# Optimization experiments

Measured on AMD Instinct MI355X. Metric: run time of the kernel, lower is better.

## Reference

```python
import jax, jax.numpy as jnp
import numpy as np

# Model constants (match init_kwargs / torchcde conventions)
B = 1024        # batch
L = 128         # number of spline knots (grid_points = 0..L-1)
C_IN = 8        # input_channels
HID = 64        # hidden_channels
MLP_H = 128     # CDEFunc hidden width
INIT_H = 20     # initial-network hidden width


def setup_inputs() -> dict:
    key = jax.random.key(0)
    ks = jax.random.split(key, 9)
    # cubic spline coeffs: (B, L-1, 4*C_IN) laid out as [a, b, c, d] per interval
    coeffs = jax.random.normal(ks[0], (B, L - 1, 4 * C_IN), dtype=jnp.float32) * 0.1
    # initial network: C_IN -> 20 -> HID (ReLU, then Tanh)
    Wi1 = jax.random.normal(ks[1], (C_IN, INIT_H), dtype=jnp.float32) / np.sqrt(C_IN)
    bi1 = jnp.zeros((INIT_H,), jnp.float32)
    Wi2 = jax.random.normal(ks[2], (INIT_H, HID), dtype=jnp.float32) / np.sqrt(INIT_H)
    bi2 = jnp.zeros((HID,), jnp.float32)
    # CDE vector field: (HID+1) -> 128 -> C_IN*HID (ReLU, then Tanh)
    W1 = jax.random.normal(ks[3], (HID + 1, MLP_H), dtype=jnp.float32) / np.sqrt(HID + 1)
    b1 = jnp.zeros((MLP_H,), jnp.float32)
    W2 = jax.random.normal(ks[4], (MLP_H, C_IN * HID), dtype=jnp.float32) / np.sqrt(MLP_H)
    b2 = jnp.zeros((C_IN * HID,), jnp.float32)
    return {"coeffs": coeffs, "Wi1": Wi1, "bi1": bi1, "Wi2": Wi2, "bi2": bi2,
            "W1": W1, "b1": b1, "W2": W2, "b2": b2}


def reference(coeffs, Wi1, bi1, Wi2, bi2, W1, b1, W2, b2):
    Lm1 = coeffs.shape[1]
    # a,b,c,d: each (B, L-1, C_IN). X(t) = a + b*f + c*f^2 + d*f^3 on interval idx,
    # dX/dt = b + 2c*f + 3d*f^2, with f = t - idx (torchcde CubicSpline convention).
    a, b, c, d = jnp.split(coeffs, 4, axis=-1)

    def dXdt(t):
        idx = jnp.clip(jnp.floor(t).astype(jnp.int32), 0, Lm1 - 1)
        fr = t - idx
        return b[:, idx] + 2.0 * c[:, idx] * fr + 3.0 * d[:, idx] * fr * fr  # (B, C_IN)

    def cde_func(t, z):
        # FFN([HID+1, 128, C_IN*HID], ReLU hidden, Tanh output) on concat(t, z)
        tz = jnp.concatenate([jnp.full((z.shape[0], 1), t, z.dtype), z], axis=1)
        h = jax.nn.relu(tz @ W1 + b1)
        return jnp.tanh(h @ W2 + b2).reshape(z.shape[0], HID, C_IN)  # (B, HID, C_IN)

    def vf(t, z):
        # dz/dt = f(t,z) @ dX/dt
        return jnp.einsum('bhc,bc->bh', cde_func(t, z), dXdt(t))

    # z0 = initial(X(t0)); X(0) = a at interval 0 with frac 0
    X0 = a[:, 0]
    z0 = jnp.tanh(jax.nn.relu(X0 @ Wi1 + bi1) @ Wi2 + bi2)  # (B, HID)

    def rk4_step(z, i):
        t = i.astype(z.dtype)
        k1 = vf(t, z)
        k2 = vf(t + 0.5, z + 0.5 * k1)
        k3 = vf(t + 0.5, z + 0.5 * k2)
        k4 = vf(t + 1.0, z + k3)
        z_new = z + (k1 + 2.0 * k2 + 2.0 * k3 + k4) / 6.0
        return z_new, z_new

    _, zs = jax.lax.scan(rk4_step, z0, jnp.arange(Lm1))  # (L-1, B, HID)
    # z evaluated at all grid points, like cdeint(t=X.grid_points): (B, L, HID)
    return jnp.concatenate([z0[None], zs], axis=0).transpose(1, 0, 2)
```

## Files before the change

kernel.cpp:

```cpp
#include <hip/hip_runtime.h>
#include <stdint.h>

#define LM1   127
#define NTHR  256

typedef _Float16 half2_t __attribute__((ext_vector_type(2)));
typedef _Float16 half8_t __attribute__((ext_vector_type(8)));
typedef float    f32x4  __attribute__((ext_vector_type(4)));

__device__ __forceinline__ float fdot2(uint32_t a, uint32_t b, float c) {
  return __builtin_amdgcn_fdot2(__builtin_bit_cast(half2_t, a),
                                __builtin_bit_cast(half2_t, b), c, false);
}
__device__ __forceinline__ uint32_t packh2(float a, float b) {
  half2_t h = {(_Float16)a, (_Float16)b};
  return __builtin_bit_cast(uint32_t, h);
}
__device__ __forceinline__ float fast_tanh(float x) {
  float e = __expf(2.0f * x);
  return 1.0f - 2.0f * __builtin_amdgcn_rcpf(e + 1.0f);
}

__global__ void __launch_bounds__(NTHR, 1) cde_kernel(
    const float* __restrict__ coeffs,
    const float* __restrict__ Wi1, const float* __restrict__ bi1,
    const float* __restrict__ Wi2, const float* __restrict__ bi2,
    const float* __restrict__ W1,  const float* __restrict__ b1,
    const float* __restrict__ W2,  const float* __restrict__ b2,
    float* __restrict__ out)
{
  __shared__ _Float16 hA[16 * 136];
  __shared__ _Float16 zsb[4 * 64];
  __shared__ float    fbuf[4 * 576];
  __shared__ float    gds[3][4][8];

  const int t    = threadIdx.x;
  const int lane = t & 63;
  const int w    = t >> 6;
  const int r    = lane & 3;
  const int hxl  = lane >> 2;
  const int hx   = w * 16 + hxl;
  const int row0 = blockIdx.x * 4;

  {
    uint32_t* h32 = (uint32_t*)hA;
    for (int u = t; u < 16 * 136 / 2; u += NTHR) h32[u] = 0u;
  }

  const int j2 = 2 * lane;
  uint32_t w1A[32], w1B[32];
  #pragma unroll 8
  for (int m = 0; m < 32; ++m) {
    w1A[m] = packh2(W1[(1 + 2 * m) * 128 + j2],     W1[(2 + 2 * m) * 128 + j2]);
    w1B[m] = packh2(W1[(1 + 2 * m) * 128 + j2 + 1], W1[(2 + 2 * m) * 128 + j2 + 1]);
  }
  const float w1t0 = W1[j2], w1t1 = W1[j2 + 1];
  const float b10  = b1[j2], b11  = b1[j2 + 1];

  float b2r[8];
  #pragma unroll
  for (int c = 0; c < 8; ++c) b2r[c] = b2[hx * 8 + c];

  half8_t bf[8][4];
  {
    const int ncol = w * 128 + (lane & 15);
    const int kq   = (lane >> 4) * 8;
    #pragma unroll
    for (int nt = 0; nt < 8; ++nt)
      #pragma unroll
      for (int kt = 0; kt < 4; ++kt)
        #pragma unroll
        for (int j = 0; j < 8; ++j)
          bf[nt][kt][j] = (_Float16)W2[(kt * 32 + kq + j) * 512 + ncol + nt * 16];
  }

  float z;
  {
    const float* cb = coeffs + (size_t)(row0 + r) * (LM1 * 32);
    float x0[8];
    #pragma unroll
    for (int c = 0; c < 8; ++c) x0[c] = cb[c];
    float acc = bi2[hx];
    for (int j = 0; j < 20; ++j) {
      float u = bi1[j];
      #pragma unroll
      for (int c = 0; c < 8; ++c) u += x0[c] * Wi1[c * 20 + j];
      u = fmaxf(u, 0.0f);
      acc += u * Wi2[j * 64 + hx];
    }
    z = fast_tanh(acc);
  }
  out[(size_t)(row0 + r) * 8192 + hx] = z;

  float* const fw = fbuf + w * 576;

  for (int i = 0; i < LM1; ++i) {
    __syncthreads();
    if (t < 32) {
      const int rg = t >> 3, cg = t & 7;
      const float* cb = coeffs + (size_t)(row0 + rg) * (LM1 * 32) + (size_t)i * 32;
      const float bb = cb[8 + cg], cc = cb[16 + cg], dd = cb[24 + cg];
      gds[0][rg][cg] = bb;
      gds[1][rg][cg] = bb + cc + 0.75f * dd;
      gds[2][rg][cg] = (i < LM1 - 1) ? cb[32 + 8 + cg]
                                     : (bb + 2.0f * cc + 3.0f * dd);
    }

    float ksum = 0.0f, kprev = 0.0f;
    #pragma unroll
    for (int s = 0; s < 4; ++s) {
      const float coef = (s == 0) ? 0.0f : (s == 3) ? 1.0f : 0.5f;
      const float ts   = (float)i + ((s == 0) ? 0.0f : (s == 3) ? 1.0f : 0.5f);
      const int   gi   = (s == 0) ? 0 : (s == 3) ? 2 : 1;

      zsb[r * 64 + hx] = (_Float16)(z + coef * kprev);
      __syncthreads();

      {
        uint32_t zz[32];
        const uint4* zq = (const uint4*)(zsb + w * 64);
        #pragma unroll
        for (int q = 0; q < 8; ++q) {
          uint4 v = zq[q];
          zz[4 * q] = v.x; zz[4 * q + 1] = v.y; zz[4 * q + 2] = v.z; zz[4 * q + 3] = v.w;
        }
        float a0 = ts * w1t0 + b10, a1 = ts * w1t1 + b11;
        float a0b = 0.0f, a1b = 0.0f;
        #pragma unroll
        for (int m = 0; m < 32; m += 2) {
          a0  = fdot2(w1A[m],     zz[m],     a0);
          a1  = fdot2(w1B[m],     zz[m],     a1);
          a0b = fdot2(w1A[m + 1], zz[m + 1], a0b);
          a1b = fdot2(w1B[m + 1], zz[m + 1], a1b);
        }
        const float h0 = fmaxf(a0 + a0b, 0.0f);
        const float h1 = fmaxf(a1 + a1b, 0.0f);
        *(uint32_t*)(hA + w * 136 + 2 * lane) = packh2(h0, h1);
      }
      __syncthreads();

      {
        uint4 afu[4];
        const _Float16* hap = hA + (lane & 15) * 136 + (lane >> 4) * 8;
        #pragma unroll
        for (int kt = 0; kt < 4; ++kt)
          afu[kt] = *(const uint4*)(hap + kt * 32);

        f32x4 dacc[8];
        #pragma unroll
        for (int np = 0; np < 4; ++np) {
          f32x4 d0 = {0.f, 0.f, 0.f, 0.f};
          f32x4 d1 = {0.f, 0.f, 0.f, 0.f};
          #pragma unroll
          for (int kt = 0; kt < 4; ++kt) {
            half8_t a = __builtin_bit_cast(half8_t, afu[kt]);
            d0 = __builtin_amdgcn_mfma_f32_16x16x32_f16(a, bf[2 * np][kt],     d0, 0, 0, 0);
            d1 = __builtin_amdgcn_mfma_f32_16x16x32_f16(a, bf[2 * np + 1][kt], d1, 0, 0, 0);
          }
          dacc[2 * np] = d0; dacc[2 * np + 1] = d1;
        }
        if (lane < 16) {
          #pragma unroll
          for (int nt = 0; nt < 8; ++nt) {
            const int cl = nt * 16 + lane;
            *(f32x4*)(fw + 4 * cl + 4 * (cl >> 3)) = dacc[nt];
          }
        }
      }
      asm volatile("s_waitcnt lgkmcnt(0)" ::: "memory");

      {
        const f32x4 ga = *(const f32x4*)&gds[gi][r][0];
        const f32x4 gb4 = *(const f32x4*)&gds[gi][r][4];
        const float gg[8] = {ga.x, ga.y, ga.z, ga.w, gb4.x, gb4.y, gb4.z, gb4.w};
        const float* fr_ = fw + 36 * hxl + r;
        float kcv = 0.0f;
        #pragma unroll
        for (int c = 0; c < 8; ++c)
          kcv += fast_tanh(fr_[4 * c] + b2r[c]) * gg[c];
        kprev = kcv;
        ksum += ((s == 1 || s == 2) ? 2.0f : 1.0f) * kcv;
      }
    }
    z += ksum * (1.0f / 6.0f);
    out[(size_t)(row0 + r) * 8192 + (size_t)(i + 1) * 64 + hx] = z;
  }
}

extern "C" void kernel_launch(void* const* d_in, const int* in_sizes, int n_in,
                              void* d_out, int out_size, void* d_ws, size_t ws_size,
                              hipStream_t stream) {
  const float* coeffs = (const float*)d_in[0];
  const float* Wi1    = (const float*)d_in[1];
  const float* bi1    = (const float*)d_in[2];
  const float* Wi2    = (const float*)d_in[3];
  const float* bi2    = (const float*)d_in[4];
  const float* W1     = (const float*)d_in[5];
  const float* b1     = (const float*)d_in[6];
  const float* W2     = (const float*)d_in[7];
  const float* b2     = (const float*)d_in[8];
  float* out          = (float*)d_out;
  (void)in_sizes; (void)n_in; (void)out_size; (void)d_ws; (void)ws_size;
  cde_kernel<<<256, NTHR, 0, stream>>>(coeffs, Wi1, bi1, Wi2, bi2,
                                       W1, b1, W2, b2, out);
}
```

Baseline: 659.2 us.

## Split work across 8 waves and compute the first layer with MFMA

Raises the block to 512 threads (8 waves), so each wave owns 64 output columns of the second GEMM and 8 hidden units for the state update. The first layer is moved from fdot2 loops to MFMA over a zero-padded 16-row z tile. The spline coefficient loads are prefetched one step ahead into double-buffered shared memory, which removes a barrier per step. Half of the lanes now sit idle during the tanh/contraction phase, and the first MFMA spends 12 of its 16 rows on padding.

Result: faster. 595.0 us (-9.7%).

```diff
diff --git a/kernel.cpp b/kernel.cpp
--- a/kernel.cpp
+++ b/kernel.cpp
@@ -1,27 +1,18 @@
 #include <hip/hip_runtime.h>
 #include <stdint.h>
 
-#define LM1   127
-#define NTHR  256
+#define LM1  127
+#define NTHR 512
 
-typedef _Float16 half2_t __attribute__((ext_vector_type(2)));
 typedef _Float16 half8_t __attribute__((ext_vector_type(8)));
-typedef float    f32x4  __attribute__((ext_vector_type(4)));
+typedef float    f32x4   __attribute__((ext_vector_type(4)));
 
-__device__ __forceinline__ float fdot2(uint32_t a, uint32_t b, float c) {
-  return __builtin_amdgcn_fdot2(__builtin_bit_cast(half2_t, a),
-                                __builtin_bit_cast(half2_t, b), c, false);
-}
-__device__ __forceinline__ uint32_t packh2(float a, float b) {
-  half2_t h = {(_Float16)a, (_Float16)b};
-  return __builtin_bit_cast(uint32_t, h);
-}
 __device__ __forceinline__ float fast_tanh(float x) {
   float e = __expf(2.0f * x);
   return 1.0f - 2.0f * __builtin_amdgcn_rcpf(e + 1.0f);
 }
 
-__global__ void __launch_bounds__(NTHR, 1) cde_kernel(
+__global__ void __launch_bounds__(NTHR, 2) cde_kernel(
     const float* __restrict__ coeffs,
     const float* __restrict__ Wi1, const float* __restrict__ bi1,
     const float* __restrict__ Wi2, const float* __restrict__ bi2,
@@ -29,53 +20,50 @@
     const float* __restrict__ W2,  const float* __restrict__ b2,
     float* __restrict__ out)
 {
-  __shared__ _Float16 hA[16 * 136];
-  __shared__ _Float16 zsb[4 * 64];
-  __shared__ float    fbuf[4 * 576];
-  __shared__ float    gds[3][4][8];
+  __shared__ _Float16 zsb[16 * 72];
+  __shared__ _Float16 hA [16 * 136];
+  __shared__ float    fwb[8][284];
+  __shared__ float    gds[2][3][4][8];
 
   const int t    = threadIdx.x;
   const int lane = t & 63;
   const int w    = t >> 6;
+  const int l15  = lane & 15;
+  const int lq   = lane >> 4;
   const int r    = lane & 3;
-  const int hxl  = lane >> 2;
-  const int hx   = w * 16 + hxl;
+  const int hxl  = (lane >> 2) & 7;
+  const int hx   = w * 8 + hxl;
   const int row0 = blockIdx.x * 4;
+  const bool owner = (lane < 32);
 
-  {
-    uint32_t* h32 = (uint32_t*)hA;
-    for (int u = t; u < 16 * 136 / 2; u += NTHR) h32[u] = 0u;
-  }
+  for (int u = t; u < 16 * 72 / 2;  u += NTHR) ((uint32_t*)zsb)[u] = 0u;
+  for (int u = t; u < 16 * 136 / 2; u += NTHR) ((uint32_t*)hA)[u]  = 0u;
 
-  const int j2 = 2 * lane;
-  uint32_t w1A[32], w1B[32];
-  #pragma unroll 8
-  for (int m = 0; m < 32; ++m) {
-    w1A[m] = packh2(W1[(1 + 2 * m) * 128 + j2],     W1[(2 + 2 * m) * 128 + j2]);
-    w1B[m] = packh2(W1[(1 + 2 * m) * 128 + j2 + 1], W1[(2 + 2 * m) * 128 + j2 + 1]);
-  }
-  const float w1t0 = W1[j2], w1t1 = W1[j2 + 1];
-  const float b10  = b1[j2], b11  = b1[j2 + 1];
+  half8_t bB[2];
+  #pragma unroll
+  for (int kt = 0; kt < 2; ++kt)
+    #pragma unroll
+    for (int j = 0; j < 8; ++j)
+      bB[kt][j] = (_Float16)W1[(1 + kt * 32 + lq * 8 + j) * 128 + w * 16 + l15];
+  const float w1t_c = W1[w * 16 + l15];
+  const float b1_c  = b1[w * 16 + l15];
+
+  half8_t bf[4][4];
+  #pragma unroll
+  for (int nt = 0; nt < 4; ++nt)
+    #pragma unroll
+    for (int kt = 0; kt < 4; ++kt)
+      #pragma unroll
+      for (int j = 0; j < 8; ++j)
+        bf[nt][kt][j] =
+            (_Float16)W2[(kt * 32 + lq * 8 + j) * 512 + w * 64 + nt * 16 + l15];
 
   float b2r[8];
   #pragma unroll
   for (int c = 0; c < 8; ++c) b2r[c] = b2[hx * 8 + c];
 
-  half8_t bf[8][4];
-  {
-    const int ncol = w * 128 + (lane & 15);
-    const int kq   = (lane >> 4) * 8;
-    #pragma unroll
-    for (int nt = 0; nt < 8; ++nt)
-      #pragma unroll
-      for (int kt = 0; kt < 4; ++kt)
-        #pragma unroll
-        for (int j = 0; j < 8; ++j)
-          bf[nt][kt][j] = (_Float16)W2[(kt * 32 + kq + j) * 512 + ncol + nt * 16];
-  }
-
-  float z;
-  {
+  float z = 0.0f;
+  if (owner) {
     const float* cb = coeffs + (size_t)(row0 + r) * (LM1 * 32);
     float x0[8];
     #pragma unroll
@@ -85,25 +73,27 @@
       float u = bi1[j];
       #pragma unroll
       for (int c = 0; c < 8; ++c) u += x0[c] * Wi1[c * 20 + j];
-      u = fmaxf(u, 0.0f);
-      acc += u * Wi2[j * 64 + hx];
+      acc += fmaxf(u, 0.0f) * Wi2[j * 64 + hx];
     }
     z = fast_tanh(acc);
+    out[(size_t)(row0 + r) * 8192 + hx] = z;
   }
-  out[(size_t)(row0 + r) * 8192 + hx] = z;
 
-  float* const fw = fbuf + w * 576;
+  const int rg = (t >> 3) & 3, cg = t & 7;
+  const float* cbp = coeffs + (size_t)(row0 + rg) * (LM1 * 32);
+  float pb = 0.f, pc = 0.f, pd = 0.f, pbn = 0.f;
+  if (t < 32) { pb = cbp[8 + cg]; pc = cbp[16 + cg]; pd = cbp[24 + cg]; pbn = cbp[40 + cg]; }
 
   for (int i = 0; i < LM1; ++i) {
-    __syncthreads();
     if (t < 32) {
-      const int rg = t >> 3, cg = t & 7;
-      const float* cb = coeffs + (size_t)(row0 + rg) * (LM1 * 32) + (size_t)i * 32;
-      const float bb = cb[8 + cg], cc = cb[16 + cg], dd = cb[24 + cg];
-      gds[0][rg][cg] = bb;
-      gds[1][rg][cg] = bb + cc + 0.75f * dd;
-      gds[2][rg][cg] = (i < LM1 - 1) ? cb[32 + 8 + cg]
-                                     : (bb + 2.0f * cc + 3.0f * dd);
+      gds[i & 1][0][rg][cg] = pb;
+      gds[i & 1][1][rg][cg] = pb + pc + 0.75f * pd;
+      gds[i & 1][2][rg][cg] = (i < LM1 - 1) ? pbn : fmaf(3.0f, pd, fmaf(2.0f, pc, pb));
+      if (i + 1 < LM1) {
+        const float* nb = cbp + (size_t)(i + 1) * 32;
+        pb = nb[8 + cg]; pc = nb[16 + cg]; pd = nb[24 + cg];
+        pbn = (i + 2 < LM1) ? nb[40 + cg] : 0.0f;
+      }
     }
 
     float ksum = 0.0f, kprev = 0.0f;
@@ -113,77 +103,67 @@
       const float ts   = (float)i + ((s == 0) ? 0.0f : (s == 3) ? 1.0f : 0.5f);
       const int   gi   = (s == 0) ? 0 : (s == 3) ? 2 : 1;
 
-      zsb[r * 64 + hx] = (_Float16)(z + coef * kprev);
+      if (owner) zsb[r * 72 + hx] = (_Float16)(z + coef * kprev);
       __syncthreads();
 
       {
-        uint32_t zz[32];
-        const uint4* zq = (const uint4*)(zsb + w * 64);
-        #pragma unroll
-        for (int q = 0; q < 8; ++q) {
-          uint4 v = zq[q];
-          zz[4 * q] = v.x; zz[4 * q + 1] = v.y; zz[4 * q + 2] = v.z; zz[4 * q + 3] = v.w;
+        half8_t a0 = *(const half8_t*)(zsb + l15 * 72 + lq * 8);
+        half8_t a1 = *(const half8_t*)(zsb + l15 * 72 + 32 + lq * 8);
+        f32x4 hd = {0.f, 0.f, 0.f, 0.f};
+        hd = __builtin_amdgcn_mfma_f32_16x16x32_f16(a0, bB[0], hd, 0, 0, 0);
+        hd = __builtin_amdgcn_mfma_f32_16x16x32_f16(a1, bB[1], hd, 0, 0, 0);
+        if (lane < 16) {
+          const float hb = fmaf(ts, w1t_c, b1_c);
+          const int col = w * 16 + lane;
+          hA[0 * 136 + col] = (_Float16)fmaxf(hd.x + hb, 0.0f);
+          hA[1 * 136 + col] = (_Float16)fmaxf(hd.y + hb, 0.0f);
+          hA[2 * 136 + col] = (_Float16)fmaxf(hd.z + hb, 0.0f);
+          hA[3 * 136 + col] = (_Float16)fmaxf(hd.w + hb, 0.0f);
         }
-        float a0 = ts * w1t0 + b10, a1 = ts * w1t1 + b11;
-        float a0b = 0.0f, a1b = 0.0f;
-        #pragma unroll
-        for (int m = 0; m < 32; m += 2) {
-          a0  = fdot2(w1A[m],     zz[m],     a0);
-          a1  = fdot2(w1B[m],     zz[m],     a1);
-          a0b = fdot2(w1A[m + 1], zz[m + 1], a0b);
-          a1b = fdot2(w1B[m + 1], zz[m + 1], a1b);
-        }
-        const float h0 = fmaxf(a0 + a0b, 0.0f);
-        const float h1 = fmaxf(a1 + a1b, 0.0f);
-        *(uint32_t*)(hA + w * 136 + 2 * lane) = packh2(h0, h1);
       }
       __syncthreads();
 
       {
-        uint4 afu[4];
-        const _Float16* hap = hA + (lane & 15) * 136 + (lane >> 4) * 8;
+        half8_t ha[4];
         #pragma unroll
         for (int kt = 0; kt < 4; ++kt)
-          afu[kt] = *(const uint4*)(hap + kt * 32);
-
-        f32x4 dacc[8];
+          ha[kt] = *(const half8_t*)(hA + l15 * 136 + kt * 32 + lq * 8);
+        f32x4 d0 = {0.f,0.f,0.f,0.f}, d1 = d0, d2 = d0, d3 = d0;
         #pragma unroll
-        for (int np = 0; np < 4; ++np) {
-          f32x4 d0 = {0.f, 0.f, 0.f, 0.f};
-          f32x4 d1 = {0.f, 0.f, 0.f, 0.f};
-          #pragma unroll
-          for (int kt = 0; kt < 4; ++kt) {
-            half8_t a = __builtin_bit_cast(half8_t, afu[kt]);
-            d0 = __builtin_amdgcn_mfma_f32_16x16x32_f16(a, bf[2 * np][kt],     d0, 0, 0, 0);
-            d1 = __builtin_amdgcn_mfma_f32_16x16x32_f16(a, bf[2 * np + 1][kt], d1, 0, 0, 0);
-          }
-          dacc[2 * np] = d0; dacc[2 * np + 1] = d1;
+        for (int kt = 0; kt < 4; ++kt) {
+          d0 = __builtin_amdgcn_mfma_f32_16x16x32_f16(ha[kt], bf[0][kt], d0, 0, 0, 0);
+          d1 = __builtin_amdgcn_mfma_f32_16x16x32_f16(ha[kt], bf[1][kt], d1, 0, 0, 0);
+          d2 = __builtin_amdgcn_mfma_f32_16x16x32_f16(ha[kt], bf[2][kt], d2, 0, 0, 0);
+          d3 = __builtin_amdgcn_mfma_f32_16x16x32_f16(ha[kt], bf[3][kt], d3, 0, 0, 0);
         }
         if (lane < 16) {
+          f32x4 dd[4] = {d0, d1, d2, d3};
           #pragma unroll
-          for (int nt = 0; nt < 8; ++nt) {
+          for (int nt = 0; nt < 4; ++nt) {
             const int cl = nt * 16 + lane;
-            *(f32x4*)(fw + 4 * cl + 4 * (cl >> 3)) = dacc[nt];
+            *(f32x4*)(&fwb[w][36 * (cl >> 3) + 4 * (cl & 7)]) = dd[nt];
           }
         }
       }
       asm volatile("s_waitcnt lgkmcnt(0)" ::: "memory");
 
-      {
-        const f32x4 ga = *(const f32x4*)&gds[gi][r][0];
-        const f32x4 gb4 = *(const f32x4*)&gds[gi][r][4];
-        const float gg[8] = {ga.x, ga.y, ga.z, ga.w, gb4.x, gb4.y, gb4.z, gb4.w};
-        const float* fr_ = fw + 36 * hxl + r;
+      if (owner) {
+        const f32x4 g0 = *(const f32x4*)&gds[i & 1][gi][r][0];
+        const f32x4 g1 = *(const f32x4*)&gds[i & 1][gi][r][4];
+        const float gg[8] = {g0.x, g0.y, g0.z, g0.w, g1.x, g1.y, g1.z, g1.w};
+        const float* fp = &fwb[w][36 * hxl + r];
         float kcv = 0.0f;
         #pragma unroll
         for (int c = 0; c < 8; ++c)
-          kcv += fast_tanh(fr_[4 * c] + b2r[c]) * gg[c];
+          kcv += fast_tanh(fp[4 * c] + b2r[c]) * gg[c];
         kprev = kcv;
         ksum += ((s == 1 || s == 2) ? 2.0f : 1.0f) * kcv;
       }
     }
-    z += ksum * (1.0f / 6.0f);
-    out[(size_t)(row0 + r) * 8192 + (size_t)(i + 1) * 64 + hx] = z;
+    if (owner) {
+      z += ksum * (1.0f / 6.0f);
+      out[(size_t)(row0 + r) * 8192 + (size_t)(i + 1) * 64 + hx] = z;
+    }
   }
 }
 
```
